# Kernel optimization log

Hardware: AMD Instinct MI355X
Metric: run time of the kernel (lower is better)

Reference implementation:

```python
import jax, jax.numpy as jnp
import numpy as np

EMB = 512
HEAD = 64
B, S = 4, 4096


def setup_inputs() -> dict:
    key = jax.random.key(0)
    kq, kk, kv, kwq, kwk, kwv = jax.random.split(key, 6)
    q = jax.random.normal(kq, (B, S, EMB), dtype=jnp.float32)
    k = jax.random.normal(kk, (B, S, EMB), dtype=jnp.float32)
    v = jax.random.normal(kv, (B, S, EMB), dtype=jnp.float32)
    # nn.Linear weights: [out_features, in_features], no bias
    sc = 1.0 / np.sqrt(EMB)
    Wq = jax.random.uniform(kwq, (HEAD, EMB), jnp.float32, -sc, sc)
    Wk = jax.random.uniform(kwk, (HEAD, EMB), jnp.float32, -sc, sc)
    Wv = jax.random.uniform(kwv, (HEAD, EMB), jnp.float32, -sc, sc)
    return {"q": q, "k": k, "v": v, "Wq": Wq, "Wk": Wk, "Wv": Wv}


def reference(q, k, v, Wq, Wk, Wv):
    scale = 1.0 / np.sqrt(HEAD).astype(np.float32)
    Q = jnp.einsum('bse,he->bsh', q, Wq)  # [B,S,HEAD]
    K = jnp.einsum('bse,he->bsh', k, Wk)
    V = jnp.einsum('bse,he->bsh', v, Wv)
    scores = jnp.einsum('bqh,bkh->bqk', Q, K) * scale  # [B,S,S]
    attn = jax.nn.softmax(scores, axis=-1)
    # dropout p=0.0 -> identity
    out = jnp.einsum('bqk,bkh->bqh', attn, V)  # [B,S,HEAD]
    return out
```

## Files before the change

kernel.cpp:

```cpp
#include <hip/hip_runtime.h>
#include <hip/hip_bf16.h>

#define EMB    512
#define HEAD   64
#define SEQ    4096
#define NB     4
#define NSPLIT 8
#define LDX    72

#define SL2E   0.18033688011112042f

typedef __bf16 bf16x8 __attribute__((ext_vector_type(8)));
typedef float  f32x4  __attribute__((ext_vector_type(4)));

__device__ inline ushort4 cvt4(float4 v) {
    __hip_bfloat16 a = __float2bfloat16(v.x), b = __float2bfloat16(v.y);
    __hip_bfloat16 c = __float2bfloat16(v.z), d = __float2bfloat16(v.w);
    ushort4 r;
    r.x = *(unsigned short*)&a; r.y = *(unsigned short*)&b;
    r.z = *(unsigned short*)&c; r.w = *(unsigned short*)&d;
    return r;
}

__device__ inline bf16x8 cvt8(float4 a, float4 b) {
    union { ushort4 u[2]; bf16x8 v; } u;
    u.u[0] = cvt4(a);
    u.u[1] = cvt4(b);
    return u.v;
}

__global__ __launch_bounds__(256) void cvtw_kernel(
    const float* __restrict__ Wq, const float* __restrict__ Wk,
    const float* __restrict__ Wv, __hip_bfloat16* __restrict__ Wc)
{
    int idx   = blockIdx.x * 256 + threadIdx.x;
    int which = idx >> 13;
    int off   = (idx & 8191) * 4;
    const float* src = (which == 0) ? Wq : (which == 1) ? Wk : Wv;
    float s = (which == 0) ? SL2E : 1.0f;
    float4 v = *(const float4*)(src + off);
    v.x *= s; v.y *= s; v.z *= s; v.w *= s;
    *(ushort4*)(Wc + which * 64 * EMB + off) = cvt4(v);
}

__global__ __launch_bounds__(256) void proj_kernel(
    const float* __restrict__ q, const float* __restrict__ k, const float* __restrict__ v,
    const __hip_bfloat16* __restrict__ Wc,
    __hip_bfloat16* __restrict__ Qo, __hip_bfloat16* __restrict__ Ko,
    __hip_bfloat16* __restrict__ Vto)
{
    const int which = blockIdx.y;
    const float* __restrict__ x = (which == 0) ? q : (which == 1) ? k : v;
    const __hip_bfloat16* __restrict__ W = Wc + which * 64 * EMB;

    const int tid  = threadIdx.x;
    const int wave = tid >> 6, lane = tid & 63;
    const int l16  = lane & 15, quad = lane >> 4;
    const int r0   = blockIdx.x * 64;
    const int myrow = r0 + wave * 16 + l16;

    const float* __restrict__ xrow = x + (size_t)myrow * EMB + quad * 8;

    const f32x4 z = {0.f, 0.f, 0.f, 0.f};
    f32x4 acc[4] = {z, z, z, z};

    float4 xr[4];
    bf16x8 wf[8];

#define LOADX(dst, e0)                                                        \
    _Pragma("unroll")                                                         \
    for (int st = 0; st < 2; ++st) {                                          \
        dst[st * 2 + 0] = *(const float4*)(xrow + (e0) + st * 32);            \
        dst[st * 2 + 1] = *(const float4*)(xrow + (e0) + st * 32 + 4);        \
    }

#define LOADW(dst, e0)                                                        \
    _Pragma("unroll")                                                         \
    for (int st = 0; st < 2; ++st)                                            \
        _Pragma("unroll")                                                     \
        for (int t = 0; t < 4; ++t)                                           \
            dst[st * 4 + t] = *(const bf16x8*)(W + (size_t)(t * 16 + l16) * EMB \
                                               + (e0) + st * 32 + quad * 8);

    LOADX(xr, 0);
    LOADW(wf, 0);

    #pragma unroll
    for (int c = 0; c < 8; ++c) {
        float4 xr2[4];
        bf16x8 wf2[8];
        if (c < 7) { LOADX(xr2, (c + 1) * 64); LOADW(wf2, (c + 1) * 64); }

        #pragma unroll
        for (int st = 0; st < 2; ++st) {
            bf16x8 a = cvt8(xr[st * 2 + 0], xr[st * 2 + 1]);
            #pragma unroll
            for (int t = 0; t < 4; ++t)
                acc[t] = __builtin_amdgcn_mfma_f32_16x16x32_bf16(a, wf[st * 4 + t], acc[t], 0, 0, 0);
        }

        if (c < 7) {
            #pragma unroll
            for (int j = 0; j < 4; ++j) xr[j] = xr2[j];
            #pragma unroll
            for (int j = 0; j < 8; ++j) wf[j] = wf2[j];
        }
    }
#undef LOADX
#undef LOADW

    #pragma unroll
    for (int t = 0; t < 4; ++t) {
        #pragma unroll
        for (int r = 0; r < 4; ++r) {
            int row = r0 + wave * 16 + quad * 4 + r;
            int h   = t * 16 + l16;
            __hip_bfloat16 val = __float2bfloat16(acc[t][r]);
            if (which == 0) {
                Qo[(size_t)row * HEAD + h] = val;
            } else if (which == 1) {
                Ko[(size_t)row * HEAD + h] = val;
            } else {
                int b = row >> 12, s = row & (SEQ - 1);
                Vto[((size_t)b * HEAD + h) * SEQ + s] = val;
            }
        }
    }
}

__global__ __launch_bounds__(256) void attn_kernel(
    const __hip_bfloat16* __restrict__ Qb, const __hip_bfloat16* __restrict__ Kb,
    const __hip_bfloat16* __restrict__ Vt, float* __restrict__ Op,
    float* __restrict__ lp)
{
    __shared__ __hip_bfloat16 Ks[64][LDX];
    __shared__ __hip_bfloat16 Vs[64][LDX];
    __shared__ __hip_bfloat16 Ps[128][LDX];

    const int tid  = threadIdx.x;
    const int wave = tid >> 6, lane = tid & 63;
    const int l16  = lane & 15, quad = lane >> 4;
    const int b    = blockIdx.y;
    const int q0   = blockIdx.x * 128;
    const int j0b  = blockIdx.z * (SEQ / NSPLIT);

    bf16x8 qf[2][2];
    #pragma unroll
    for (int s = 0; s < 2; ++s) {
        const __hip_bfloat16* qrow =
            Qb + ((size_t)b * SEQ + q0 + wave * 32 + s * 16 + l16) * HEAD + quad * 8;
        qf[s][0] = *(const bf16x8*)(qrow);
        qf[s][1] = *(const bf16x8*)(qrow + 32);
    }

    const f32x4 z = {0.f, 0.f, 0.f, 0.f};
    f32x4 oacc[2][4] = {{z, z, z, z}, {z, z, z, z}};
    f32x4 lacc[2] = {z, z};

    const __hip_bfloat16 one_bf = __float2bfloat16(1.0f);
    bf16x8 ones;
    #pragma unroll
    for (int j = 0; j < 8; ++j) ones[j] = *(const __bf16*)&one_bf;

    for (int jt = 0; jt < SEQ / NSPLIT; jt += 64) {
        const int j0 = j0b + jt;
        __syncthreads();
        for (int i = tid; i < 512; i += 256) {
            int r = i >> 3, c8 = (i & 7) * 8;
            *(uint4*)&Ks[r][c8] =
                *(const uint4*)(Kb + ((size_t)b * SEQ + j0 + r) * HEAD + c8);
            *(uint4*)&Vs[r][c8] =
                *(const uint4*)(Vt + ((size_t)b * HEAD + r) * SEQ + j0 + c8);
        }
        __syncthreads();

        f32x4 sacc[2][4] = {{z, z, z, z}, {z, z, z, z}};
        #pragma unroll
        for (int st = 0; st < 2; ++st) {
            #pragma unroll
            for (int t = 0; t < 4; ++t) {
                bf16x8 kf = *(const bf16x8*)&Ks[t * 16 + l16][st * 32 + quad * 8];
                #pragma unroll
                for (int s = 0; s < 2; ++s)
                    sacc[s][t] = __builtin_amdgcn_mfma_f32_16x16x32_bf16(qf[s][st], kf, sacc[s][t], 0, 0, 0);
            }
        }

        #pragma unroll
        for (int s = 0; s < 2; ++s)
            #pragma unroll
            for (int r = 0; r < 4; ++r)
                #pragma unroll
                for (int t = 0; t < 4; ++t) {
                    float p = __builtin_amdgcn_exp2f(sacc[s][t][r]);
                    Ps[wave * 32 + s * 16 + quad * 4 + r][t * 16 + l16] = __float2bfloat16(p);
                }

        #pragma unroll
        for (int s = 0; s < 2; ++s) {
            #pragma unroll
            for (int st = 0; st < 2; ++st) {
                bf16x8 pf = *(const bf16x8*)&Ps[wave * 32 + s * 16 + l16][st * 32 + quad * 8];
                lacc[s] = __builtin_amdgcn_mfma_f32_16x16x32_bf16(pf, ones, lacc[s], 0, 0, 0);
                #pragma unroll
                for (int t = 0; t < 4; ++t) {
                    bf16x8 vf = *(const bf16x8*)&Vs[t * 16 + l16][st * 32 + quad * 8];
                    oacc[s][t] = __builtin_amdgcn_mfma_f32_16x16x32_bf16(pf, vf, oacc[s][t], 0, 0, 0);
                }
            }
        }
    }

    const size_t pb = (size_t)(blockIdx.z * NB + b) * SEQ;
    #pragma unroll
    for (int s = 0; s < 2; ++s) {
        const size_t row0 = pb + q0 + wave * 32 + s * 16 + quad * 4;
        if (l16 == 0) {
            #pragma unroll
            for (int r = 0; r < 4; ++r)
                lp[row0 + r] = lacc[s][r];
        }
        #pragma unroll
        for (int t = 0; t < 4; ++t)
            #pragma unroll
            for (int r = 0; r < 4; ++r)
                Op[(row0 + r) * HEAD + t * 16 + l16] = oacc[s][t][r];
    }
}

__global__ __launch_bounds__(256) void merge_kernel(
    const float* __restrict__ Op, const float* __restrict__ lp,
    float* __restrict__ out)
{
    int idx = blockIdx.x * 256 + threadIdx.x;
    int bq  = idx >> 4;
    int c4  = (idx & 15) * 4;
    float4 acc = {0.f, 0.f, 0.f, 0.f};
    float  l   = 0.f;
    #pragma unroll
    for (int s = 0; s < NSPLIT; ++s) {
        float4 o = *(const float4*)(Op + ((size_t)s * NB * SEQ + bq) * HEAD + c4);
        acc.x += o.x; acc.y += o.y; acc.z += o.z; acc.w += o.w;
        l += lp[(size_t)s * NB * SEQ + bq];
    }
    float inv = 1.f / l;
    float4 r = {acc.x * inv, acc.y * inv, acc.z * inv, acc.w * inv};
    *(float4*)(out + (size_t)bq * HEAD + c4) = r;
}

extern "C" void kernel_launch(void* const* d_in, const int* in_sizes, int n_in,
                              void* d_out, int out_size, void* d_ws, size_t ws_size,
                              hipStream_t stream) {
    const float* q  = (const float*)d_in[0];
    const float* k  = (const float*)d_in[1];
    const float* v  = (const float*)d_in[2];
    const float* Wq = (const float*)d_in[3];
    const float* Wk = (const float*)d_in[4];
    const float* Wv = (const float*)d_in[5];
    float* out = (float*)d_out;

    __hip_bfloat16* Qb = (__hip_bfloat16*)d_ws;
    __hip_bfloat16* Kb = Qb + (size_t)NB * SEQ * HEAD;
    __hip_bfloat16* Vt = Kb + (size_t)NB * SEQ * HEAD;
    __hip_bfloat16* Wc = Vt + (size_t)NB * SEQ * HEAD;
    float* Op = (float*)(Wc + 3 * 64 * EMB);
    float* lp = Op + (size_t)NSPLIT * NB * SEQ * HEAD;

    cvtw_kernel<<<96, 256, 0, stream>>>(Wq, Wk, Wv, Wc);

    dim3 pgrid(NB * SEQ / 64, 3);
    proj_kernel<<<pgrid, dim3(256), 0, stream>>>(q, k, v, Wc, Qb, Kb, Vt);

    dim3 agrid(SEQ / 128, NB, NSPLIT);
    attn_kernel<<<agrid, dim3(256), 0, stream>>>(Qb, Kb, Vt, Op, lp);

    merge_kernel<<<(NB * SEQ * 16) / 256, dim3(256), 0, stream>>>(Op, lp, out);
}
```

Measured before the change: 186.5 us.

## Split projection reduction dimension across waves with shared-memory partial sum

```diff
diff --git a/kernel.cpp b/kernel.cpp
--- a/kernel.cpp
+++ b/kernel.cpp
@@ -49,80 +49,76 @@
     __hip_bfloat16* __restrict__ Qo, __hip_bfloat16* __restrict__ Ko,
     __hip_bfloat16* __restrict__ Vto)
 {
+    __shared__ float Pp[3][16][65];
+
     const int which = blockIdx.y;
     const float* __restrict__ x = (which == 0) ? q : (which == 1) ? k : v;
     const __hip_bfloat16* __restrict__ W = Wc + which * 64 * EMB;
 
     const int tid  = threadIdx.x;
-    const int wave = tid >> 6, lane = tid & 63;
+    const int kh   = tid >> 6;
+    const int lane = tid & 63;
     const int l16  = lane & 15, quad = lane >> 4;
-    const int r0   = blockIdx.x * 64;
-    const int myrow = r0 + wave * 16 + l16;
-
-    const float* __restrict__ xrow = x + (size_t)myrow * EMB + quad * 8;
+    const int r0   = blockIdx.x * 16;
+    const int kbase = kh * 128;
+
+    const float* __restrict__ xrow = x + (size_t)(r0 + l16) * EMB + kbase + quad * 8;
+    const __hip_bfloat16* __restrict__ wbase = W + kbase + quad * 8;
 
     const f32x4 z = {0.f, 0.f, 0.f, 0.f};
     f32x4 acc[4] = {z, z, z, z};
 
-    float4 xr[4];
-    bf16x8 wf[8];
-
-#define LOADX(dst, e0)                                                        \
-    _Pragma("unroll")                                                         \
-    for (int st = 0; st < 2; ++st) {                                          \
-        dst[st * 2 + 0] = *(const float4*)(xrow + (e0) + st * 32);            \
-        dst[st * 2 + 1] = *(const float4*)(xrow + (e0) + st * 32 + 4);        \
-    }
-
-#define LOADW(dst, e0)                                                        \
-    _Pragma("unroll")                                                         \
-    for (int st = 0; st < 2; ++st)                                            \
-        _Pragma("unroll")                                                     \
-        for (int t = 0; t < 4; ++t)                                           \
-            dst[st * 4 + t] = *(const bf16x8*)(W + (size_t)(t * 16 + l16) * EMB \
-                                               + (e0) + st * 32 + quad * 8);
-
-    LOADX(xr, 0);
-    LOADW(wf, 0);
-
-    #pragma unroll
-    for (int c = 0; c < 8; ++c) {
-        float4 xr2[4];
-        bf16x8 wf2[8];
-        if (c < 7) { LOADX(xr2, (c + 1) * 64); LOADW(wf2, (c + 1) * 64); }
-
+    float4 xr[8];
+    #pragma unroll
+    for (int c = 0; c < 2; ++c)
         #pragma unroll
         for (int st = 0; st < 2; ++st) {
-            bf16x8 a = cvt8(xr[st * 2 + 0], xr[st * 2 + 1]);
-            #pragma unroll
-            for (int t = 0; t < 4; ++t)
-                acc[t] = __builtin_amdgcn_mfma_f32_16x16x32_bf16(a, wf[st * 4 + t], acc[t], 0, 0, 0);
-        }
-
-        if (c < 7) {
-            #pragma unroll
-            for (int j = 0; j < 4; ++j) xr[j] = xr2[j];
-            #pragma unroll
-            for (int j = 0; j < 8; ++j) wf[j] = wf2[j];
-        }
-    }
-#undef LOADX
-#undef LOADW
-
-    #pragma unroll
-    for (int t = 0; t < 4; ++t) {
-        #pragma unroll
-        for (int r = 0; r < 4; ++r) {
-            int row = r0 + wave * 16 + quad * 4 + r;
-            int h   = t * 16 + l16;
-            __hip_bfloat16 val = __float2bfloat16(acc[t][r]);
-            if (which == 0) {
-                Qo[(size_t)row * HEAD + h] = val;
-            } else if (which == 1) {
-                Ko[(size_t)row * HEAD + h] = val;
-            } else {
-                int b = row >> 12, s = row & (SEQ - 1);
-                Vto[((size_t)b * HEAD + h) * SEQ + s] = val;
+            xr[(c * 2 + st) * 2 + 0] = *(const float4*)(xrow + c * 64 + st * 32);
+            xr[(c * 2 + st) * 2 + 1] = *(const float4*)(xrow + c * 64 + st * 32 + 4);
+        }
+
+    #pragma unroll
+    for (int c = 0; c < 2; ++c) {
+        #pragma unroll
+        for (int st = 0; st < 2; ++st) {
+            bf16x8 a = cvt8(xr[(c * 2 + st) * 2 + 0], xr[(c * 2 + st) * 2 + 1]);
+            #pragma unroll
+            for (int t = 0; t < 4; ++t) {
+                bf16x8 wfr = *(const bf16x8*)(wbase + (size_t)(t * 16 + l16) * EMB
+                                              + c * 64 + st * 32);
+                acc[t] = __builtin_amdgcn_mfma_f32_16x16x32_bf16(a, wfr, acc[t], 0, 0, 0);
+            }
+        }
+    }
+
+    if (kh != 0) {
+        #pragma unroll
+        for (int t = 0; t < 4; ++t)
+            #pragma unroll
+            for (int r = 0; r < 4; ++r)
+                Pp[kh - 1][quad * 4 + r][t * 16 + l16] = acc[t][r];
+    }
+    __syncthreads();
+    if (kh == 0) {
+        #pragma unroll
+        for (int t = 0; t < 4; ++t) {
+            #pragma unroll
+            for (int r = 0; r < 4; ++r) {
+                float s = acc[t][r]
+                        + Pp[0][quad * 4 + r][t * 16 + l16]
+                        + Pp[1][quad * 4 + r][t * 16 + l16]
+                        + Pp[2][quad * 4 + r][t * 16 + l16];
+                int row = r0 + quad * 4 + r;
+                int h   = t * 16 + l16;
+                __hip_bfloat16 val = __float2bfloat16(s);
+                if (which == 0) {
+                    Qo[(size_t)row * HEAD + h] = val;
+                } else if (which == 1) {
+                    Ko[(size_t)row * HEAD + h] = val;
+                } else {
+                    int b = row >> 12, ss = row & (SEQ - 1);
+                    Vto[((size_t)b * HEAD + h) * SEQ + ss] = val;
+                }
             }
         }
     }
@@ -268,7 +264,7 @@
 
     cvtw_kernel<<<96, 256, 0, stream>>>(Wq, Wk, Wv, Wc);
 
-    dim3 pgrid(NB * SEQ / 64, 3);
+    dim3 pgrid(NB * SEQ / 16, 3);
     proj_kernel<<<pgrid, dim3(256), 0, stream>>>(q, k, v, Wc, Qb, Kb, Vt);
 
     dim3 agrid(SEQ / 128, NB, NSPLIT);
```

Result: slower. 192.1 us (+3.0%).
